# Kernel optimization log

Measured on AMD Instinct MI355X. Metric: run time of the kernel, lower is better.

## Reference

```python
import jax, jax.numpy as jnp
import numpy as np

N = 150000      # nodes
E_AST = 300000  # ast edges
E_CFG = 250000  # cfg edges
D = 256         # in_size = out_size
N_STEPS = 2


def _gru(a, h, Wih, Whh, bih, bhh):
    # torch.nn.GRUCell semantics: input a, hidden h
    gi = a @ Wih.T + bih            # [N, 3D]
    gh = h @ Whh.T + bhh            # [N, 3D]
    ir, iz, i_n = jnp.split(gi, 3, axis=-1)
    hr, hz, h_n = jnp.split(gh, 3, axis=-1)
    r = jax.nn.sigmoid(ir + hr)
    z = jax.nn.sigmoid(iz + hz)
    n = jnp.tanh(i_n + r * h_n)
    return (1.0 - z) * n + z * h


def _gated_graph_conv(h, src, dst, W, b, Wih, Whh, bih, bhh):
    # DGL GatedGraphConv, n_etypes=1, in_feats == out_feats
    n_nodes = h.shape[0]
    for _ in range(N_STEPS):
        m = (h @ W.T + b)[src]                                   # per-edge gather [E, D]
        a = jax.ops.segment_sum(m, dst, num_segments=n_nodes)    # scatter-sum to dst
        h = _gru(a, h, Wih, Whh, bih, bhh)
    return h


def setup_inputs() -> dict:
    key = jax.random.key(0)
    ks = jax.random.split(key, 16)
    s = 1.0 / np.sqrt(D)
    inp = {
        'nodes': jax.random.normal(ks[0], (N, D), jnp.float32),
        'ast_src': jax.random.randint(ks[1], (E_AST,), 0, N),
        'ast_dst': jax.random.randint(ks[2], (E_AST,), 0, N),
        'cfg_src': jax.random.randint(ks[3], (E_CFG,), 0, N),
        'cfg_dst': jax.random.randint(ks[4], (E_CFG,), 0, N),
        'W_ast': jax.random.normal(ks[5], (D, D), jnp.float32) * s,
        'b_ast': jnp.zeros((D,), jnp.float32),
        'Wih_ast': jax.random.normal(ks[6], (3 * D, D), jnp.float32) * s,
        'Whh_ast': jax.random.normal(ks[7], (3 * D, D), jnp.float32) * s,
        'bih_ast': jnp.zeros((3 * D,), jnp.float32),
        'bhh_ast': jnp.zeros((3 * D,), jnp.float32),
        'w1': jax.random.normal(ks[8], (D, 2 * D), jnp.float32) * (1.0 / np.sqrt(2 * D)),
        'b1': jnp.zeros((D,), jnp.float32),
        'W_cpg': jax.random.normal(ks[9], (D, D), jnp.float32) * s,
        'b_cpg': jnp.zeros((D,), jnp.float32),
        'Wih_cpg': jax.random.normal(ks[10], (3 * D, D), jnp.float32) * s,
        'Whh_cpg': jax.random.normal(ks[11], (3 * D, D), jnp.float32) * s,
        'bih_cpg': jnp.zeros((3 * D,), jnp.float32),
        'bhh_cpg': jnp.zeros((3 * D,), jnp.float32),
        'w2': jax.random.normal(ks[12], (D, 2 * D), jnp.float32) * (1.0 / np.sqrt(2 * D)),
        'b2': jnp.zeros((D,), jnp.float32),
    }
    return inp


def reference(nodes, ast_src, ast_dst, cfg_src, cfg_dst,
              W_ast, b_ast, Wih_ast, Whh_ast, bih_ast, bhh_ast,
              w1, b1,
              W_cpg, b_cpg, Wih_cpg, Whh_cpg, bih_cpg, bhh_cpg,
              w2, b2):
    # ast branch: GatedGraphConv -> concat with input -> fn_1
    h_ast = _gated_graph_conv(nodes, ast_src, ast_dst,
                              W_ast, b_ast, Wih_ast, Whh_ast, bih_ast, bhh_ast)
    hiddens = jnp.concatenate([h_ast, nodes], axis=-1) @ w1.T + b1   # [N, D]
    # cpg branch: GatedGraphConv -> concat with hiddens -> fn_2
    h_cpg = _gated_graph_conv(hiddens, cfg_src, cfg_dst,
                              W_cpg, b_cpg, Wih_cpg, Whh_cpg, bih_cpg, bhh_cpg)
    logits = jnp.concatenate([h_cpg, hiddens], axis=-1) @ w2.T + b2  # [N, D]
    return logits
```

## Files before the change

kernel.cpp:

```cpp
#include <hip/hip_runtime.h>

typedef _Float16 f16;
typedef _Float16 f16x8 __attribute__((ext_vector_type(8)));
typedef float f32x16 __attribute__((ext_vector_type(16)));

__device__ __forceinline__ f16x8 cvt8p(const float* p) {
  float4 a = *(const float4*)p;
  float4 b = *(const float4*)(p + 4);
  f16x8 v;
  v[0] = (f16)a.x; v[1] = (f16)a.y; v[2] = (f16)a.z; v[3] = (f16)a.w;
  v[4] = (f16)b.x; v[5] = (f16)b.y; v[6] = (f16)b.z; v[7] = (f16)b.w;
  return v;
}

__device__ __forceinline__ void gload16(const void* g, void* l) {
  __builtin_amdgcn_global_load_lds((const __attribute__((address_space(1))) unsigned int*)g,
                                   (__attribute__((address_space(3))) unsigned int*)l, 16, 0, 0);
}

__device__ __forceinline__ float sigm(float x) {
  return __builtin_amdgcn_rcpf(1.f + __expf(-x));
}
__device__ __forceinline__ float tanh_(float x) {
  x = fminf(15.f, fmaxf(-15.f, x));
  float e = __expf(2.f * x);
  return 1.f - 2.f * __builtin_amdgcn_rcpf(e + 1.f);
}


__global__ void k_cvt8(const float* __restrict__ x, f16* __restrict__ y, long n) {
  long i = ((long)blockIdx.x * blockDim.x + threadIdx.x) * 8;
  long stride = (long)gridDim.x * blockDim.x * 8;
  for (; i < n; i += stride) *(f16x8*)(y + i) = cvt8p(x + i);
}

__global__ void k_wc2(const float* __restrict__ Wih, const float* __restrict__ W,
                      unsigned char* __restrict__ dstb) {
  int j = blockIdx.x;
  int k = threadIdx.x;
  float s = 0.f;
  for (int c = 0; c < 256; ++c) s = fmaf(Wih[j * 256 + c], W[c * 256 + k], s);
  int g = j >> 8, hcol = j & 255;
  int hb = hcol >> 5, trow = hcol & 31;
  int kc = k >> 6, kl = k & 63;
  int slot = (kl >> 3) ^ (trow & 7);
  size_t byte = (size_t)hb * 98304 + (size_t)kc * 12288 +
                (size_t)(g * 32 + trow) * 128 + slot * 16 + (kl & 7) * 2;
  *(f16*)(dstb + byte) = (f16)s;
}

__global__ void k_whh2(const float* __restrict__ Whh, unsigned char* __restrict__ dstb) {
  int j = blockIdx.x;
  int k = threadIdx.x;
  float s = Whh[j * 256 + k];
  int g = j >> 8, hcol = j & 255;
  int hb = hcol >> 5, trow = hcol & 31;
  int kc = 4 + (k >> 6), kl = k & 63;
  int slot = (kl >> 3) ^ (trow & 7);
  size_t byte = (size_t)hb * 98304 + (size_t)kc * 12288 +
                (size_t)(g * 32 + trow) * 128 + slot * 16 + (kl & 7) * 2;
  *(f16*)(dstb + byte) = (f16)s;
}

__global__ void k_prepw(const float* __restrict__ w, unsigned char* __restrict__ dstb) {
  int j = blockIdx.x;
  int cg = j >> 6, R = j & 63;
  for (int k = threadIdx.x; k < 512; k += 256) {
    int kc = k >> 6, kl = k & 63;
    int slot = (kl >> 3) ^ (R & 7);
    size_t byte = (size_t)(cg * 8 + kc) * 8192 + (size_t)R * 128 + slot * 16 + (kl & 7) * 2;
    *(f16*)(dstb + byte) = (f16)w[j * 512 + k];
  }
}

__global__ void k_v(const float* __restrict__ Wih, const float* __restrict__ b,
                    float* __restrict__ v) {
  int j = blockIdx.x * blockDim.x + threadIdx.x;
  if (j < 768) {
    float s = 0.f;
    for (int c = 0; c < 256; ++c) s = fmaf(Wih[j * 256 + c], b[c], s);
    v[j] = s;
  }
}

__global__ void k_hist(const int* __restrict__ dst, int* __restrict__ cnt, int E) {
  int e = blockIdx.x * 256 + threadIdx.x;
  if (e < E) atomicAdd(&cnt[dst[e]], 1);
}

__global__ void k_scan1(const int* __restrict__ deg, int* __restrict__ rowptr,
                        int* __restrict__ bsum, int n) {
  __shared__ int buf[256];
  int i = blockIdx.x * 256 + threadIdx.x;
  int v = (i < n) ? deg[i] : 0;
  buf[threadIdx.x] = v;
  __syncthreads();
  for (int off = 1; off < 256; off <<= 1) {
    int t = 0;
    if ((int)threadIdx.x >= off) t = buf[threadIdx.x - off];
    __syncthreads();
    buf[threadIdx.x] += t;
    __syncthreads();
  }
  if (i < n) rowptr[i] = buf[threadIdx.x] - v;
  if (threadIdx.x == 255) bsum[blockIdx.x] = buf[255];
}

__global__ void k_scan2(int* __restrict__ bsum, int nb) {
  __shared__ int buf[1024];
  int v = ((int)threadIdx.x < nb) ? bsum[threadIdx.x] : 0;
  buf[threadIdx.x] = v;
  __syncthreads();
  for (int off = 1; off < 1024; off <<= 1) {
    int t = 0;
    if ((int)threadIdx.x >= off) t = buf[threadIdx.x - off];
    __syncthreads();
    buf[threadIdx.x] += t;
    __syncthreads();
  }
  if ((int)threadIdx.x < nb) bsum[threadIdx.x] = buf[threadIdx.x] - v;
}

__global__ void k_scan3(int* __restrict__ rowptr, const int* __restrict__ bsum,
                        int n, int E) {
  int i = blockIdx.x * 256 + threadIdx.x;
  if (i < n) rowptr[i] += bsum[blockIdx.x];
  if (i == n) rowptr[n] = E;
}

__global__ void k_fill(const int* __restrict__ src, const int* __restrict__ dst,
                       const int* __restrict__ rowptr, int* __restrict__ cnt,
                       int* __restrict__ esrc, int E) {
  int e = blockIdx.x * 256 + threadIdx.x;
  if (e < E) {
    int d = dst[e];
    int r = atomicAdd(&cnt[d], 1);
    esrc[rowptr[d] + r] = src[e];
  }
}

__global__ void k_gather(const f16* __restrict__ h, const int* __restrict__ rowptr,
                         const int* __restrict__ esrc, f16* __restrict__ ag, int n) {
  int g = threadIdx.x >> 5, l = threadIdx.x & 31;
  int node = blockIdx.x * 8 + g;
  if (node >= n) return;
  int e0 = rowptr[node], e1 = rowptr[node + 1];
  float acc[8];
#pragma unroll
  for (int j = 0; j < 8; ++j) acc[j] = 0.f;
  int e = e0;
  for (; e + 2 <= e1; e += 2) {
    int s0 = esrc[e], s1 = esrc[e + 1];
    f16x8 hv0 = *(const f16x8*)(h + (long)s0 * 256 + l * 8);
    f16x8 hv1 = *(const f16x8*)(h + (long)s1 * 256 + l * 8);
#pragma unroll
    for (int j = 0; j < 8; ++j) acc[j] += (float)hv0[j] + (float)hv1[j];
  }
  if (e < e1) {
    int s0 = esrc[e];
    f16x8 hv0 = *(const f16x8*)(h + (long)s0 * 256 + l * 8);
#pragma unroll
    for (int j = 0; j < 8; ++j) acc[j] += (float)hv0[j];
  }
  f16x8 o;
#pragma unroll
  for (int j = 0; j < 8; ++j) o[j] = (f16)acc[j];
  *(f16x8*)(ag + (long)node * 256 + l * 8) = o;
}

__global__ __launch_bounds__(256, 4) void k_gru(
    const f16* __restrict__ ag, const f16* __restrict__ hin,
    const unsigned char* __restrict__ wprep, const float* __restrict__ bih,
    const float* __restrict__ bhh, const float* __restrict__ vv,
    const int* __restrict__ rowptr, f16* __restrict__ hout, int n, int nper) {
  __shared__ unsigned char SM[24576 + 512];
  float* Ds = (float*)(SM + 24576);
  int bid = blockIdx.x;
  int w = (bid & 7) * nper + (bid >> 3);
  int rt = w >> 3, hb = w & 7;
  int row0 = rt * 128;
  int tid = threadIdx.x, lane = tid & 63, wid = tid >> 6;
  int l31 = lane & 31, hi = lane >> 5;
  const unsigned char* wb = wprep + (size_t)hb * 98304;

  auto stage = [&](int c, unsigned char* dst) {
    const unsigned char* s0 = wb + (size_t)c * 12288;
#pragma unroll
    for (int i = 0; i < 3; ++i) {
      int r = i * 4 + wid;
      gload16(s0 + r * 1024 + lane * 16, dst + r * 1024);
    }
  };

  int arow = row0 + wid * 32 + l31;
  const f16* agp = ag + (size_t)arow * 256 + hi * 8;
  const f16* hp = hin + (size_t)arow * 256 + hi * 8;

  f16x8 a[4];
  auto loadA = [&](const f16* p, int koff) {
#pragma unroll
    for (int ks = 0; ks < 4; ++ks)
      a[ks] = *(const f16x8*)(p + koff + ks * 16);
  };
  int sl0 = l31 & 7;
  auto runC = [&](const unsigned char* Bb, f32x16& aR, f32x16& aZ, f32x16& aN) {
#pragma unroll
    for (int ks = 0; ks < 4; ++ks) {
      int sl = (ks * 2 + hi) ^ sl0;
      const unsigned char* base = Bb + sl * 16;
      f16x8 b0 = *(const f16x8*)(base + (0 * 32 + l31) * 128);
      aR = __builtin_amdgcn_mfma_f32_32x32x16_f16(a[ks], b0, aR, 0, 0, 0);
      f16x8 b1 = *(const f16x8*)(base + (1 * 32 + l31) * 128);
      aZ = __builtin_amdgcn_mfma_f32_32x32x16_f16(a[ks], b1, aZ, 0, 0, 0);
      f16x8 b2 = *(const f16x8*)(base + (2 * 32 + l31) * 128);
      aN = __builtin_amdgcn_mfma_f32_32x32x16_f16(a[ks], b2, aN, 0, 0, 0);
    }
  };

  f32x16 accR, accZ, accNI, accNH;
#pragma unroll
  for (int j = 0; j < 16; ++j) { accR[j] = 0.f; accZ[j] = 0.f; accNI[j] = 0.f; accNH[j] = 0.f; }

  stage(0, SM);
  loadA(agp, 0);
  if (tid < 128) {
    int grow = row0 + tid;
    Ds[tid] = (grow < n) ? (float)(rowptr[grow + 1] - rowptr[grow]) : 0.f;
  }
  __syncthreads();

  stage(1, SM + 12288);
  runC(SM, accR, accZ, accNI);
  loadA(agp, 64);
  __syncthreads();
  stage(2, SM);
  runC(SM + 12288, accR, accZ, accNI);
  loadA(agp, 128);
  __syncthreads();
  stage(3, SM + 12288);
  runC(SM, accR, accZ, accNI);
  loadA(agp, 192);
  __syncthreads();
  stage(4, SM);
  runC(SM + 12288, accR, accZ, accNI);
  loadA(hp, 0);
  __syncthreads();
  stage(5, SM + 12288);
  runC(SM, accR, accZ, accNH);
  loadA(hp, 64);
  __syncthreads();
  stage(6, SM);
  runC(SM + 12288, accR, accZ, accNH);
  loadA(hp, 128);
  __syncthreads();
  stage(7, SM + 12288);
  runC(SM, accR, accZ, accNH);
  loadA(hp, 192);
  __syncthreads();
  runC(SM + 12288, accR, accZ, accNH);

  int gcol = hb * 32 + l31;
  float br = bih[gcol] + bhh[gcol];
  float bz = bih[256 + gcol] + bhh[256 + gcol];
  float bi_n = bih[512 + gcol], bh_n = bhh[512 + gcol];
  float vr = vv[gcol], vz = vv[256 + gcol], vn = vv[512 + gcol];
  int wrow = wid * 32;

#pragma unroll
  for (int rg = 0; rg < 16; ++rg) {
    int crow = (rg & 3) + 8 * (rg >> 2) + 4 * hi;
    int grow = row0 + wrow + crow;
    float dg = Ds[wrow + crow];
    float hold = (float)hin[(size_t)grow * 256 + gcol];
    float r = sigm(accR[rg] + br + dg * vr);
    float z = sigm(accZ[rg] + bz + dg * vz);
    float nn = tanh_(accNI[rg] + bi_n + dg * vn + r * (accNH[rg] + bh_n));
    if (grow < n)
      hout[(size_t)grow * 256 + gcol] = (f16)((1.f - z) * nn + z * hold);
  }
}

template <int WMODE>
__global__ __launch_bounds__(256, 4) void k_fn(
    const f16* __restrict__ hb, const f16* __restrict__ base16,
    const unsigned char* __restrict__ wp, const float* __restrict__ bias,
    float* __restrict__ out32, f16* __restrict__ out16, int n, int nper) {
  __shared__ unsigned char SM[16384];
  int bid = blockIdx.x;
  int w = (bid & 7) * nper + (bid >> 3);
  int rt = w >> 2, cg = w & 3;
  int row0 = rt * 128;
  int tid = threadIdx.x, lane = tid & 63, wid = tid >> 6;
  int l31 = lane & 31, hi = lane >> 5;
  const unsigned char* wb = wp + (size_t)cg * 65536;

  auto stage = [&](int c, unsigned char* dst) {
    const unsigned char* s0 = wb + (size_t)c * 8192;
#pragma unroll
    for (int i = 0; i < 2; ++i) {
      int r = i * 4 + wid;
      gload16(s0 + r * 1024 + lane * 16, dst + r * 1024);
    }
  };

  int arow = row0 + wid * 32 + l31;
  const f16* hbp = hb + (size_t)arow * 256 + hi * 8;
  const f16* bsp = base16 + (size_t)arow * 256 + hi * 8;

  f16x8 a[4];
  auto loadA = [&](const f16* p, int koff) {
#pragma unroll
    for (int ks = 0; ks < 4; ++ks)
      a[ks] = *(const f16x8*)(p + koff + ks * 16);
  };
  int sl0 = l31 & 7;

  f32x16 acc0, acc1;
#pragma unroll
  for (int j = 0; j < 16; ++j) { acc0[j] = 0.f; acc1[j] = 0.f; }

  auto runC = [&](const unsigned char* Bb) {
#pragma unroll
    for (int ks = 0; ks < 4; ++ks) {
      int sl = (ks * 2 + hi) ^ sl0;
      const unsigned char* base = Bb + sl * 16;
      f16x8 b0 = *(const f16x8*)(base + (0 + l31) * 128);
      acc0 = __builtin_amdgcn_mfma_f32_32x32x16_f16(a[ks], b0, acc0, 0, 0, 0);
      f16x8 b1 = *(const f16x8*)(base + (32 + l31) * 128);
      acc1 = __builtin_amdgcn_mfma_f32_32x32x16_f16(a[ks], b1, acc1, 0, 0, 0);
    }
  };

  stage(0, SM);
  loadA(hbp, 0);
  __syncthreads();
  stage(1, SM + 8192); runC(SM);        loadA(hbp, 64);  __syncthreads();
  stage(2, SM);        runC(SM + 8192); loadA(hbp, 128); __syncthreads();
  stage(3, SM + 8192); runC(SM);        loadA(hbp, 192); __syncthreads();
  stage(4, SM);        runC(SM + 8192); loadA(bsp, 0);   __syncthreads();
  stage(5, SM + 8192); runC(SM);        loadA(bsp, 64);  __syncthreads();
  stage(6, SM);        runC(SM + 8192); loadA(bsp, 128); __syncthreads();
  stage(7, SM + 8192); runC(SM);        loadA(bsp, 192); __syncthreads();
  runC(SM + 8192);

  int colb = cg * 64;
  float bb0 = bias[colb + l31], bb1 = bias[colb + 32 + l31];
#pragma unroll
  for (int rg = 0; rg < 16; ++rg) {
    int grow = row0 + wid * 32 + (rg & 3) + 8 * (rg >> 2) + 4 * hi;
    if (grow < n) {
      if (WMODE == 0) {
        out32[(size_t)grow * 256 + colb + l31] = acc0[rg] + bb0;
        out32[(size_t)grow * 256 + colb + 32 + l31] = acc1[rg] + bb1;
      } else {
        out16[(size_t)grow * 256 + colb + l31] = (f16)(acc0[rg] + bb0);
        out16[(size_t)grow * 256 + colb + 32 + l31] = (f16)(acc1[rg] + bb1);
      }
    }
  }
}

extern "C" void kernel_launch(void* const* d_in, const int* in_sizes, int n_in,
                              void* d_out, int out_size, void* d_ws, size_t ws_size,
                              hipStream_t stream) {
  const float* nodes = (const float*)d_in[0];
  const int* asrc = (const int*)d_in[1];
  const int* adst = (const int*)d_in[2];
  const int* csrc = (const int*)d_in[3];
  const int* cdst = (const int*)d_in[4];
  const float* W_ast = (const float*)d_in[5];
  const float* b_ast = (const float*)d_in[6];
  const float* Wih_a = (const float*)d_in[7];
  const float* Whh_a = (const float*)d_in[8];
  const float* bih_a = (const float*)d_in[9];
  const float* bhh_a = (const float*)d_in[10];
  const float* w1 = (const float*)d_in[11];
  const float* b1 = (const float*)d_in[12];
  const float* W_cpg = (const float*)d_in[13];
  const float* b_cpg = (const float*)d_in[14];
  const float* Wih_c = (const float*)d_in[15];
  const float* Whh_c = (const float*)d_in[16];
  const float* bih_c = (const float*)d_in[17];
  const float* bhh_c = (const float*)d_in[18];
  const float* w2 = (const float*)d_in[19];
  const float* b2 = (const float*)d_in[20];
  float* out = (float*)d_out;

  const int N = in_sizes[0] / 256;
  const int EA = in_sizes[1];
  const int EC = in_sizes[3];
  const long ND = (long)N * 256;

  char* ws = (char*)d_ws;
  size_t off = 0;
  auto carve = [&](size_t bytes) -> char* {
    char* p = ws + off;
    off += (bytes + 255) & ~(size_t)255;
    return p;
  };
  f16* h0 = (f16*)carve(ND * 2);
  f16* h1 = (f16*)carve(ND * 2);
  f16* ag = (f16*)carve(ND * 2);
  f16* nd16 = (f16*)carve(ND * 2);
  unsigned char* wpA = (unsigned char*)carve(786432);
  unsigned char* wpC = (unsigned char*)carve(786432);
  unsigned char* w1p = (unsigned char*)carve(262144);
  unsigned char* w2p = (unsigned char*)carve(262144);
  float* vA = (float*)carve(768 * 4);
  float* vC = (float*)carve(768 * 4);
  int* rowptr = (int*)carve((size_t)(N + 1) * 4);
  int* cnt = (int*)carve((size_t)N * 4);
  int* esrc = (int*)carve((size_t)(EA > EC ? EA : EC) * 4);
  int* bsum = (int*)carve(1024 * 4);
  (void)ws_size; (void)n_in; (void)out_size;

  const int NRB = (N + 127) / 128;
  const int GGRID = NRB * 8;
  const int FGRID = NRB * 4;
  const int SBLK = (N + 255) / 256;
  {
    int blocks = (int)((ND / 8 + 255) / 256);
    if (blocks > 2048) blocks = 2048;
    k_cvt8<<<blocks, 256, 0, stream>>>(nodes, nd16, ND);
  }

  k_wc2<<<768, 256, 0, stream>>>(Wih_a, W_ast, wpA);
  k_wc2<<<768, 256, 0, stream>>>(Wih_c, W_cpg, wpC);
  k_whh2<<<768, 256, 0, stream>>>(Whh_a, wpA);
  k_whh2<<<768, 256, 0, stream>>>(Whh_c, wpC);
  k_prepw<<<256, 256, 0, stream>>>(w1, w1p);
  k_prepw<<<256, 256, 0, stream>>>(w2, w2p);
  k_v<<<3, 256, 0, stream>>>(Wih_a, b_ast, vA);
  k_v<<<3, 256, 0, stream>>>(Wih_c, b_cpg, vC);

  auto run_branch = [&](const int* src, const int* dst, int E, const unsigned char* wprep,
                        const float* bih, const float* bhh, const float* v,
                        const f16* hstart, f16* t1, f16* t2) {
    hipMemsetAsync(cnt, 0, (size_t)N * 4, stream);
    k_hist<<<(E + 255) / 256, 256, 0, stream>>>(dst, cnt, E);
    k_scan1<<<SBLK, 256, 0, stream>>>(cnt, rowptr, bsum, N);
    k_scan2<<<1, 1024, 0, stream>>>(bsum, SBLK);
    k_scan3<<<SBLK, 256, 0, stream>>>(rowptr, bsum, N, E);
    hipMemsetAsync(cnt, 0, (size_t)N * 4, stream);
    k_fill<<<(E + 255) / 256, 256, 0, stream>>>(src, dst, rowptr, cnt, esrc, E);
    k_gather<<<(N + 7) / 8, 256, 0, stream>>>(hstart, rowptr, esrc, ag, N);
    k_gru<<<GGRID, 256, 0, stream>>>(ag, hstart, wprep, bih, bhh, v, rowptr, t1, N, NRB);
    k_gather<<<(N + 7) / 8, 256, 0, stream>>>(t1, rowptr, esrc, ag, N);
    k_gru<<<GGRID, 256, 0, stream>>>(ag, t1, wprep, bih, bhh, v, rowptr, t2, N, NRB);
  };

  run_branch(asrc, adst, EA, wpA, bih_a, bhh_a, vA, nd16, h1, h0);
  k_fn<1><<<FGRID, 256, 0, stream>>>(h0, nd16, w1p, b1, nullptr, h1, N, FGRID / 8);
  run_branch(csrc, cdst, EC, wpC, bih_c, bhh_c, vC, h1, h0, nd16);
  k_fn<0><<<FGRID, 256, 0, stream>>>(nd16, h1, w2p, b2, out, nullptr, N, FGRID / 8);
}
```

Before: 1.311 ms.

## Read GRU weights directly from global in MFMA-fragment layout, drop LDS staging

The fused GRU weights are prepacked so that each lane's B fragment for every k-step and gate is a contiguous 16-byte load. The GRU kernel then reads them straight from global/L2 instead of staging through double-buffered LDS with barriers. This removes the LDS traffic and the per-chunk __syncthreads, at the cost of more global loads per wave and less latency hiding. Separately, the edge-fill pass now counts down from the histogram with atomicSub, which makes the second memset of the count array unnecessary; a single memset per run replaces the two per branch.

```diff
diff --git a/kernel.cpp b/kernel.cpp
--- a/kernel.cpp
+++ b/kernel.cpp
@@ -34,7 +34,7 @@
   for (; i < n; i += stride) *(f16x8*)(y + i) = cvt8p(x + i);
 }
 
-__global__ void k_wc2(const float* __restrict__ Wih, const float* __restrict__ W,
+__global__ void k_wc3(const float* __restrict__ Wih, const float* __restrict__ W,
                       unsigned char* __restrict__ dstb) {
   int j = blockIdx.x;
   int k = threadIdx.x;
@@ -42,23 +42,25 @@
   for (int c = 0; c < 256; ++c) s = fmaf(Wih[j * 256 + c], W[c * 256 + k], s);
   int g = j >> 8, hcol = j & 255;
   int hb = hcol >> 5, trow = hcol & 31;
-  int kc = k >> 6, kl = k & 63;
-  int slot = (kl >> 3) ^ (trow & 7);
-  size_t byte = (size_t)hb * 98304 + (size_t)kc * 12288 +
-                (size_t)(g * 32 + trow) * 128 + slot * 16 + (kl & 7) * 2;
+  int ch = k >> 6, kl = k & 63;
+  int ks = kl >> 4, hi2 = (kl >> 3) & 1, el = kl & 7;
+  int lane = hi2 * 32 + trow;
+  size_t byte = (size_t)hb * 98304 + (size_t)ch * 12288 +
+                (size_t)(ks * 3 + g) * 1024 + lane * 16 + el * 2;
   *(f16*)(dstb + byte) = (f16)s;
 }
 
-__global__ void k_whh2(const float* __restrict__ Whh, unsigned char* __restrict__ dstb) {
+__global__ void k_whh3(const float* __restrict__ Whh, unsigned char* __restrict__ dstb) {
   int j = blockIdx.x;
   int k = threadIdx.x;
   float s = Whh[j * 256 + k];
   int g = j >> 8, hcol = j & 255;
   int hb = hcol >> 5, trow = hcol & 31;
-  int kc = 4 + (k >> 6), kl = k & 63;
-  int slot = (kl >> 3) ^ (trow & 7);
-  size_t byte = (size_t)hb * 98304 + (size_t)kc * 12288 +
-                (size_t)(g * 32 + trow) * 128 + slot * 16 + (kl & 7) * 2;
+  int ch = 4 + (k >> 6), kl = k & 63;
+  int ks = kl >> 4, hi2 = (kl >> 3) & 1, el = kl & 7;
+  int lane = hi2 * 32 + trow;
+  size_t byte = (size_t)hb * 98304 + (size_t)ch * 12288 +
+                (size_t)(ks * 3 + g) * 1024 + lane * 16 + el * 2;
   *(f16*)(dstb + byte) = (f16)s;
 }
 
@@ -134,8 +136,8 @@
   int e = blockIdx.x * 256 + threadIdx.x;
   if (e < E) {
     int d = dst[e];
-    int r = atomicAdd(&cnt[d], 1);
-    esrc[rowptr[d] + r] = src[e];
+    int r = atomicSub(&cnt[d], 1);
+    esrc[rowptr[d] + r - 1] = src[e];
   }
 }
 
@@ -173,24 +175,14 @@
     const unsigned char* __restrict__ wprep, const float* __restrict__ bih,
     const float* __restrict__ bhh, const float* __restrict__ vv,
     const int* __restrict__ rowptr, f16* __restrict__ hout, int n, int nper) {
-  __shared__ unsigned char SM[24576 + 512];
-  float* Ds = (float*)(SM + 24576);
+  __shared__ float Ds[128];
   int bid = blockIdx.x;
   int w = (bid & 7) * nper + (bid >> 3);
   int rt = w >> 3, hb = w & 7;
   int row0 = rt * 128;
   int tid = threadIdx.x, lane = tid & 63, wid = tid >> 6;
   int l31 = lane & 31, hi = lane >> 5;
-  const unsigned char* wb = wprep + (size_t)hb * 98304;
-
-  auto stage = [&](int c, unsigned char* dst) {
-    const unsigned char* s0 = wb + (size_t)c * 12288;
-#pragma unroll
-    for (int i = 0; i < 3; ++i) {
-      int r = i * 4 + wid;
-      gload16(s0 + r * 1024 + lane * 16, dst + r * 1024);
-    }
-  };
+  const unsigned char* bp = wprep + (size_t)hb * 98304 + lane * 16;
 
   int arow = row0 + wid * 32 + l31;
   const f16* agp = ag + (size_t)arow * 256 + hi * 8;
@@ -202,26 +194,24 @@
     for (int ks = 0; ks < 4; ++ks)
       a[ks] = *(const f16x8*)(p + koff + ks * 16);
   };
-  int sl0 = l31 & 7;
-  auto runC = [&](const unsigned char* Bb, f32x16& aR, f32x16& aZ, f32x16& aN) {
+
+  f32x16 accR, accZ, accNI, accNH;
+#pragma unroll
+  for (int j = 0; j < 16; ++j) { accR[j] = 0.f; accZ[j] = 0.f; accNI[j] = 0.f; accNH[j] = 0.f; }
+
+  auto runC = [&](int c, f32x16& aN) {
+    const unsigned char* cb = bp + (size_t)c * 12288;
 #pragma unroll
     for (int ks = 0; ks < 4; ++ks) {
-      int sl = (ks * 2 + hi) ^ sl0;
-      const unsigned char* base = Bb + sl * 16;
-      f16x8 b0 = *(const f16x8*)(base + (0 * 32 + l31) * 128);
-      aR = __builtin_amdgcn_mfma_f32_32x32x16_f16(a[ks], b0, aR, 0, 0, 0);
-      f16x8 b1 = *(const f16x8*)(base + (1 * 32 + l31) * 128);
-      aZ = __builtin_amdgcn_mfma_f32_32x32x16_f16(a[ks], b1, aZ, 0, 0, 0);
-      f16x8 b2 = *(const f16x8*)(base + (2 * 32 + l31) * 128);
+      f16x8 b0 = *(const f16x8*)(cb + (ks * 3 + 0) * 1024);
+      accR = __builtin_amdgcn_mfma_f32_32x32x16_f16(a[ks], b0, accR, 0, 0, 0);
+      f16x8 b1 = *(const f16x8*)(cb + (ks * 3 + 1) * 1024);
+      accZ = __builtin_amdgcn_mfma_f32_32x32x16_f16(a[ks], b1, accZ, 0, 0, 0);
+      f16x8 b2 = *(const f16x8*)(cb + (ks * 3 + 2) * 1024);
       aN = __builtin_amdgcn_mfma_f32_32x32x16_f16(a[ks], b2, aN, 0, 0, 0);
     }
   };
 
-  f32x16 accR, accZ, accNI, accNH;
-#pragma unroll
-  for (int j = 0; j < 16; ++j) { accR[j] = 0.f; accZ[j] = 0.f; accNI[j] = 0.f; accNH[j] = 0.f; }
-
-  stage(0, SM);
   loadA(agp, 0);
   if (tid < 128) {
     int grow = row0 + tid;
@@ -229,35 +219,14 @@
   }
   __syncthreads();
 
-  stage(1, SM + 12288);
-  runC(SM, accR, accZ, accNI);
-  loadA(agp, 64);
-  __syncthreads();
-  stage(2, SM);
-  runC(SM + 12288, accR, accZ, accNI);
-  loadA(agp, 128);
-  __syncthreads();
-  stage(3, SM + 12288);
-  runC(SM, accR, accZ, accNI);
-  loadA(agp, 192);
-  __syncthreads();
-  stage(4, SM);
-  runC(SM + 12288, accR, accZ, accNI);
-  loadA(hp, 0);
-  __syncthreads();
-  stage(5, SM + 12288);
-  runC(SM, accR, accZ, accNH);
-  loadA(hp, 64);
-  __syncthreads();
-  stage(6, SM);
-  runC(SM + 12288, accR, accZ, accNH);
-  loadA(hp, 128);
-  __syncthreads();
-  stage(7, SM + 12288);
-  runC(SM, accR, accZ, accNH);
-  loadA(hp, 192);
-  __syncthreads();
-  runC(SM + 12288, accR, accZ, accNH);
+  runC(0, accNI); loadA(agp, 64);
+  runC(1, accNI); loadA(agp, 128);
+  runC(2, accNI); loadA(agp, 192);
+  runC(3, accNI); loadA(hp, 0);
+  runC(4, accNH); loadA(hp, 64);
+  runC(5, accNH); loadA(hp, 128);
+  runC(6, accNH); loadA(hp, 192);
+  runC(7, accNH);
 
   int gcol = hb * 32 + l31;
   float br = bih[gcol] + bhh[gcol];
@@ -424,24 +393,23 @@
     k_cvt8<<<blocks, 256, 0, stream>>>(nodes, nd16, ND);
   }
 
-  k_wc2<<<768, 256, 0, stream>>>(Wih_a, W_ast, wpA);
-  k_wc2<<<768, 256, 0, stream>>>(Wih_c, W_cpg, wpC);
-  k_whh2<<<768, 256, 0, stream>>>(Whh_a, wpA);
-  k_whh2<<<768, 256, 0, stream>>>(Whh_c, wpC);
+  k_wc3<<<768, 256, 0, stream>>>(Wih_a, W_ast, wpA);
+  k_wc3<<<768, 256, 0, stream>>>(Wih_c, W_cpg, wpC);
+  k_whh3<<<768, 256, 0, stream>>>(Whh_a, wpA);
+  k_whh3<<<768, 256, 0, stream>>>(Whh_c, wpC);
   k_prepw<<<256, 256, 0, stream>>>(w1, w1p);
   k_prepw<<<256, 256, 0, stream>>>(w2, w2p);
   k_v<<<3, 256, 0, stream>>>(Wih_a, b_ast, vA);
   k_v<<<3, 256, 0, stream>>>(Wih_c, b_cpg, vC);
+  hipMemsetAsync(cnt, 0, (size_t)N * 4, stream);
 
   auto run_branch = [&](const int* src, const int* dst, int E, const unsigned char* wprep,
                         const float* bih, const float* bhh, const float* v,
                         const f16* hstart, f16* t1, f16* t2) {
-    hipMemsetAsync(cnt, 0, (size_t)N * 4, stream);
     k_hist<<<(E + 255) / 256, 256, 0, stream>>>(dst, cnt, E);
     k_scan1<<<SBLK, 256, 0, stream>>>(cnt, rowptr, bsum, N);
     k_scan2<<<1, 1024, 0, stream>>>(bsum, SBLK);
     k_scan3<<<SBLK, 256, 0, stream>>>(rowptr, bsum, N, E);
-    hipMemsetAsync(cnt, 0, (size_t)N * 4, stream);
     k_fill<<<(E + 255) / 256, 256, 0, stream>>>(src, dst, rowptr, cnt, esrc, E);
     k_gather<<<(N + 7) / 8, 256, 0, stream>>>(hstart, rowptr, esrc, ag, N);
     k_gru<<<GGRID, 256, 0, stream>>>(ag, hstart, wprep, bih, bhh, v, rowptr, t1, N, NRB);
```

Result: slower. 1.581 ms (+20.5%).

## Triple-buffer GRU weight staging with explicit vmcnt waits; reuse histogram counts in fill

Applied to the files above, without the earlier changes.

The GRU kernel moves from double-buffered to triple-buffered LDS staging of weight chunks, keeping two chunks in flight. It ping-pongs the A-operand registers and replaces __syncthreads with raw s_barrier plus manual vmcnt waits and sched barriers, so global loads can overlap the MFMA work. Launch bounds drop from 4 to 3 blocks per SM to make room for the larger LDS footprint and extra registers. Separately, k_fill counts down from the histogram with atomicSub, so the per-branch cnt memsets become one memset up front. The hand-tuned vmcnt counts are fragile if the compiler reorders or merges loads.

```diff
diff --git a/kernel.cpp b/kernel.cpp
--- a/kernel.cpp
+++ b/kernel.cpp
@@ -3,6 +3,10 @@
 typedef _Float16 f16;
 typedef _Float16 f16x8 __attribute__((ext_vector_type(8)));
 typedef float f32x16 __attribute__((ext_vector_type(16)));
+
+#define WAITV(N) asm volatile("s_waitcnt vmcnt(" #N ")" ::: "memory")
+#define FENCE() __builtin_amdgcn_sched_barrier(0)
+#define BARRIER() __builtin_amdgcn_s_barrier()
 
 __device__ __forceinline__ f16x8 cvt8p(const float* p) {
   float4 a = *(const float4*)p;
@@ -134,8 +138,8 @@
   int e = blockIdx.x * 256 + threadIdx.x;
   if (e < E) {
     int d = dst[e];
-    int r = atomicAdd(&cnt[d], 1);
-    esrc[rowptr[d] + r] = src[e];
+    int r = atomicSub(&cnt[d], 1);
+    esrc[rowptr[d] + r - 1] = src[e];
   }
 }
 
@@ -168,13 +172,13 @@
   *(f16x8*)(ag + (long)node * 256 + l * 8) = o;
 }
 
-__global__ __launch_bounds__(256, 4) void k_gru(
+__global__ __launch_bounds__(256, 3) void k_gru(
     const f16* __restrict__ ag, const f16* __restrict__ hin,
     const unsigned char* __restrict__ wprep, const float* __restrict__ bih,
     const float* __restrict__ bhh, const float* __restrict__ vv,
     const int* __restrict__ rowptr, f16* __restrict__ hout, int n, int nper) {
-  __shared__ unsigned char SM[24576 + 512];
-  float* Ds = (float*)(SM + 24576);
+  __shared__ unsigned char SM[3 * 12288 + 512];
+  float* Ds = (float*)(SM + 36864);
   int bid = blockIdx.x;
   int w = (bid & 7) * nper + (bid >> 3);
   int rt = w >> 3, hb = w & 7;
@@ -183,8 +187,9 @@
   int l31 = lane & 31, hi = lane >> 5;
   const unsigned char* wb = wprep + (size_t)hb * 98304;
 
-  auto stage = [&](int c, unsigned char* dst) {
+  auto stage = [&](int c, int bufi) {
     const unsigned char* s0 = wb + (size_t)c * 12288;
+    unsigned char* dst = SM + (size_t)bufi * 12288;
 #pragma unroll
     for (int i = 0; i < 3; ++i) {
       int r = i * 4 + wid;
@@ -196,14 +201,15 @@
   const f16* agp = ag + (size_t)arow * 256 + hi * 8;
   const f16* hp = hin + (size_t)arow * 256 + hi * 8;
 
-  f16x8 a[4];
-  auto loadA = [&](const f16* p, int koff) {
+  f16x8 a0[4], a1[4];
+  auto loadAInto = [&](f16x8(&a)[4], const f16* p, int koff) {
 #pragma unroll
     for (int ks = 0; ks < 4; ++ks)
       a[ks] = *(const f16x8*)(p + koff + ks * 16);
   };
   int sl0 = l31 & 7;
-  auto runC = [&](const unsigned char* Bb, f32x16& aR, f32x16& aZ, f32x16& aN) {
+  auto runC = [&](const f16x8(&a)[4], const unsigned char* Bb,
+                  f32x16& aR, f32x16& aZ, f32x16& aN) {
 #pragma unroll
     for (int ks = 0; ks < 4; ++ks) {
       int sl = (ks * 2 + hi) ^ sl0;
@@ -221,43 +227,43 @@
 #pragma unroll
   for (int j = 0; j < 16; ++j) { accR[j] = 0.f; accZ[j] = 0.f; accNI[j] = 0.f; accNH[j] = 0.f; }
 
-  stage(0, SM);
-  loadA(agp, 0);
+  stage(0, 0);
+  stage(1, 1);
+  loadAInto(a0, agp, 0);
   if (tid < 128) {
     int grow = row0 + tid;
     Ds[tid] = (grow < n) ? (float)(rowptr[grow + 1] - rowptr[grow]) : 0.f;
   }
   __syncthreads();
 
-  stage(1, SM + 12288);
-  runC(SM, accR, accZ, accNI);
-  loadA(agp, 64);
-  __syncthreads();
-  stage(2, SM);
-  runC(SM + 12288, accR, accZ, accNI);
-  loadA(agp, 128);
-  __syncthreads();
-  stage(3, SM + 12288);
-  runC(SM, accR, accZ, accNI);
-  loadA(agp, 192);
-  __syncthreads();
-  stage(4, SM);
-  runC(SM + 12288, accR, accZ, accNI);
-  loadA(hp, 0);
-  __syncthreads();
-  stage(5, SM + 12288);
-  runC(SM, accR, accZ, accNH);
-  loadA(hp, 64);
-  __syncthreads();
-  stage(6, SM);
-  runC(SM + 12288, accR, accZ, accNH);
-  loadA(hp, 128);
-  __syncthreads();
-  stage(7, SM + 12288);
-  runC(SM, accR, accZ, accNH);
-  loadA(hp, 192);
-  __syncthreads();
-  runC(SM + 12288, accR, accZ, accNH);
+  stage(2, 2);
+  runC(a0, SM, accR, accZ, accNI);
+  loadAInto(a1, agp, 64);
+  FENCE(); BARRIER(); FENCE();
+  stage(3, 0);
+  runC(a1, SM + 12288, accR, accZ, accNI);
+  loadAInto(a0, agp, 128);
+  WAITV(11); FENCE(); BARRIER(); FENCE();
+  stage(4, 1);
+  runC(a0, SM + 24576, accR, accZ, accNI);
+  loadAInto(a1, agp, 192);
+  WAITV(11); FENCE(); BARRIER(); FENCE();
+  stage(5, 2);
+  runC(a1, SM, accR, accZ, accNI);
+  loadAInto(a0, hp, 0);
+  WAITV(11); FENCE(); BARRIER(); FENCE();
+  stage(6, 0);
+  runC(a0, SM + 12288, accR, accZ, accNH);
+  loadAInto(a1, hp, 64);
+  WAITV(11); FENCE(); BARRIER(); FENCE();
+  stage(7, 1);
+  runC(a1, SM + 24576, accR, accZ, accNH);
+  loadAInto(a0, hp, 128);
+  WAITV(11); FENCE(); BARRIER(); FENCE();
+  runC(a0, SM, accR, accZ, accNH);
+  loadAInto(a1, hp, 192);
+  WAITV(8); FENCE(); BARRIER(); FENCE();
+  runC(a1, SM + 12288, accR, accZ, accNH);
 
   int gcol = hb * 32 + l31;
   float br = bih[gcol] + bhh[gcol];
@@ -432,16 +438,15 @@
   k_prepw<<<256, 256, 0, stream>>>(w2, w2p);
   k_v<<<3, 256, 0, stream>>>(Wih_a, b_ast, vA);
   k_v<<<3, 256, 0, stream>>>(Wih_c, b_cpg, vC);
+  hipMemsetAsync(cnt, 0, (size_t)N * 4, stream);
 
   auto run_branch = [&](const int* src, const int* dst, int E, const unsigned char* wprep,
                         const float* bih, const float* bhh, const float* v,
                         const f16* hstart, f16* t1, f16* t2) {
-    hipMemsetAsync(cnt, 0, (size_t)N * 4, stream);
     k_hist<<<(E + 255) / 256, 256, 0, stream>>>(dst, cnt, E);
     k_scan1<<<SBLK, 256, 0, stream>>>(cnt, rowptr, bsum, N);
     k_scan2<<<1, 1024, 0, stream>>>(bsum, SBLK);
     k_scan3<<<SBLK, 256, 0, stream>>>(rowptr, bsum, N, E);
-    hipMemsetAsync(cnt, 0, (size_t)N * 4, stream);
     k_fill<<<(E + 255) / 256, 256, 0, stream>>>(src, dst, rowptr, cnt, esrc, E);
     k_gather<<<(N + 7) / 8, 256, 0, stream>>>(hstart, rowptr, esrc, ag, N);
     k_gru<<<GGRID, 256, 0, stream>>>(ag, hstart, wprep, bih, bhh, v, rowptr, t1, N, NRB);
```

Result: no change. 1.305 ms (-0.5%).
